# Kernel tuning notes

Hardware: AMD Instinct MI355X
Metric: run time of the kernel (lower is better)

The kernel has to match this reference:

```python
import jax, jax.numpy as jnp
import numpy as np

L, E, K, H, I = 2, 8, 2, 1024, 2048  # stack_size, num_experts, top_k, hidden, intermediate
B, S = 1, 2048


def setup_inputs() -> dict:
    key = jax.random.key(0)
    k0, k1, k2, k3 = jax.random.split(key, 4)
    hidden_states = jax.random.normal(k0, (B, S, H), dtype=jnp.float32)
    router_w = jax.random.normal(k1, (L, H, E), dtype=jnp.float32) * 0.02
    gate_up_proj = jax.random.normal(k2, (L, E, H, 2 * I), dtype=jnp.float32) * (1.0 / np.sqrt(H))
    down_proj = jax.random.normal(k3, (L, E, I, H), dtype=jnp.float32) * (1.0 / np.sqrt(I))
    return {"hidden_states": hidden_states, "router_w": router_w,
            "gate_up_proj": gate_up_proj, "down_proj": down_proj}


def _moe_layer(x, rw, gu_w, dn_w):
    # x: [T,H]; one MoE block: RouterTopK(softmax) + full-capacity top-k GLU expert MLPs
    logits = x @ rw                                   # [T,E] router linear (fp32)
    aff = jax.nn.softmax(logits, axis=-1)
    vals, idx = jax.lax.top_k(aff, K)                 # [T,K]
    vals = vals / jnp.sum(vals, axis=-1, keepdims=True)  # normalize_top_k_affinities=True
    T = x.shape[0]
    # sparse combine weights [T,E]: normalized affinity on chosen experts, 0 elsewhere
    combine = jnp.zeros((T, E), x.dtype).at[jnp.arange(T)[:, None], idx].set(vals)
    gu = jnp.einsum('th,ehi->eti', x, gu_w)           # [E,T,2I] fused gate+up per expert
    gate, up = gu[..., :I], gu[..., I:]
    act = jax.nn.silu(gate) * up                      # GLU with silu
    eo = jnp.einsum('eti,eih->eth', act, dn_w)        # [E,T,H] down proj
    out = jnp.einsum('eth,te->th', eo, combine)       # combine over experts
    return out, logits


def reference(hidden_states, router_w, gate_up_proj, down_proj):
    Bx, Sx, Hx = hidden_states.shape
    x = hidden_states.reshape(-1, Hx)                 # [T,H]
    logits_all = []
    for l in range(L):                                # fixed small stack of layers
        x, logits = _moe_layer(x, router_w[l], gate_up_proj[l], down_proj[l])
        logits_all.append(logits)
    return x.reshape(Bx, Sx, Hx), jnp.stack(logits_all)  # output, [L,T,E] router logits
```

## Files before the change

kernel.cpp:

```cpp
#include <hip/hip_runtime.h>
#include <cstdint>
#include <cstddef>

constexpr int Lc = 2, Ec = 8, Hc = 1024, Ic = 2048, Tc = 2048;

typedef __bf16 bf16x8 __attribute__((ext_vector_type(8)));
typedef float f32x4 __attribute__((ext_vector_type(4)));

__device__ __forceinline__ unsigned short f2bf(float f) {
  unsigned u = __builtin_bit_cast(unsigned, f);
  u = (u + 0x7fffu + ((u >> 16) & 1u)) >> 16;
  return (unsigned short)u;
}
__device__ __forceinline__ float bf2f(unsigned short h) {
  unsigned u = (unsigned)h << 16;
  return __builtin_bit_cast(float, u);
}
__device__ __forceinline__ bf16x8 ldfrag(const unsigned short* p) {
  return __builtin_bit_cast(bf16x8, *(const uint4*)p);
}
__device__ __forceinline__ void gl2lds(const unsigned short* g, void* lds) {
  __builtin_amdgcn_global_load_lds(
      (const __attribute__((address_space(1))) void*)g,
      (__attribute__((address_space(3))) void*)lds, 16, 0, 0);
}

__global__ void router_kernel(const float* __restrict__ x, const float* __restrict__ rw,
                              float* __restrict__ logits) {
  const int t = blockIdx.x;
  const int tid = threadIdx.x;
  float acc[Ec];
#pragma unroll
  for (int e = 0; e < Ec; ++e) acc[e] = 0.f;
  const float* xr = x + (size_t)t * Hc;
  for (int h = tid; h < Hc; h += 256) {
    const float xv = xr[h];
    const float* w = rw + (size_t)h * Ec;
#pragma unroll
    for (int e = 0; e < Ec; ++e) acc[e] += xv * w[e];
  }
  __shared__ float red[256][Ec];
#pragma unroll
  for (int e = 0; e < Ec; ++e) red[tid][e] = acc[e];
  __syncthreads();
  for (int s = 128; s > 0; s >>= 1) {
    if (tid < s) {
#pragma unroll
      for (int e = 0; e < Ec; ++e) red[tid][e] += red[tid + s][e];
    }
    __syncthreads();
  }
  if (tid < Ec) logits[(size_t)t * Ec + tid] = red[0][tid];
}

__global__ void topk_kernel(const float* __restrict__ logits, int* __restrict__ cnt,
                            int* __restrict__ tokList, float* __restrict__ wList) {
  const int t = blockIdx.x * blockDim.x + threadIdx.x;
  if (t >= Tc) return;
  float l[Ec];
#pragma unroll
  for (int e = 0; e < Ec; ++e) l[e] = logits[(size_t)t * Ec + e];
  float b0 = -3.4e38f, b1 = -3.4e38f;
  int i0 = 0, i1 = 0;
#pragma unroll
  for (int e = 0; e < Ec; ++e) {
    if (l[e] > b0) { b1 = b0; i1 = i0; b0 = l[e]; i0 = e; }
    else if (l[e] > b1) { b1 = l[e]; i1 = e; }
  }
  const float w0 = 1.f / (1.f + expf(b1 - b0));
  const float w1 = 1.f - w0;
  int p0 = atomicAdd(&cnt[i0], 1);
  tokList[i0 * Tc + p0] = t;
  wList[i0 * Tc + p0] = w0;
  int p1 = atomicAdd(&cnt[i1], 1);
  tokList[i1 * Tc + p1] = t;
  wList[i1 * Tc + p1] = w1;
}

__global__ void offsets_kernel(const int* __restrict__ cnt, int* __restrict__ off) {
  if (threadIdx.x == 0) {
    int s = 0;
    for (int e = 0; e < Ec; ++e) { off[e] = s; s += cnt[e]; }
  }
}

__global__ void convert_kernel(const float* __restrict__ x, unsigned short* __restrict__ xh,
                               unsigned short* __restrict__ xl) {
  const int i = blockIdx.x * 256 + threadIdx.x;
  const float v = x[i];
  const unsigned short h = f2bf(v);
  xh[i] = h;
  xl[i] = f2bf(v - bf2f(h));
}

template <bool SPLIT>
__global__ __launch_bounds__(256) void wconv_kernel(const float* __restrict__ src,
                                                    unsigned short* __restrict__ dh,
                                                    unsigned short* __restrict__ dl,
                                                    int K, int N) {
  const int e = blockIdx.z;
  const int n0 = blockIdx.x * 64;
  const int k0 = blockIdx.y * 64;
  const int NB = N >> 6, KS = K >> 5;
  src += (size_t)e * K * N;

  __shared__ unsigned short lh[64][66];
  __shared__ unsigned short ll[SPLIT ? 64 : 1][66];
  const int tid = threadIdx.x;

  {
    const int r = tid >> 2, cg = (tid & 3) * 16;
    const float* sp = src + (size_t)(k0 + r) * N + n0 + cg;
#pragma unroll
    for (int i = 0; i < 16; i += 4) {
      const float4 v = *(const float4*)(sp + i);
      const float f[4] = {v.x, v.y, v.z, v.w};
#pragma unroll
      for (int j = 0; j < 4; ++j) {
        const unsigned short h = f2bf(f[j]);
        lh[r][cg + i + j] = h;
        if constexpr (SPLIT) ll[r][cg + i + j] = f2bf(f[j] - bf2f(h));
      }
    }
  }
  __syncthreads();
  {
    const int ksl = tid >> 7, q = (tid >> 5) & 3, n2 = (tid & 31) * 2;
    const int kb = ksl * 32 + q * 8;
    union { unsigned short s[16]; uint4 u[2]; } oh, ol;
#pragma unroll
    for (int s = 0; s < 2; ++s)
#pragma unroll
      for (int i = 0; i < 8; ++i) {
        oh.s[s * 8 + i] = lh[kb + i][n2 + s];
        if constexpr (SPLIT) ol.s[s * 8 + i] = ll[kb + i][n2 + s];
      }
    const size_t cb =
        (((size_t)e * NB + (n0 >> 6)) * KS + (k0 >> 5) + ksl) * 2048 + q * 512 + n2 * 8;
    *(uint4*)(dh + cb) = oh.u[0];
    *(uint4*)(dh + cb + 8) = oh.u[1];
    if constexpr (SPLIT) {
      *(uint4*)(dl + cb) = ol.u[0];
      *(uint4*)(dl + cb + 8) = ol.u[1];
    }
  }
}

template <bool SPLIT>
__global__ __launch_bounds__(256) void gateup_kernel(
    const unsigned short* __restrict__ xh, const unsigned short* __restrict__ xl,
    const unsigned short* __restrict__ gwSh, const unsigned short* __restrict__ gwSl,
    const int* __restrict__ cnt, const int* __restrict__ off,
    const int* __restrict__ tokList, unsigned short* __restrict__ actH,
    unsigned short* __restrict__ actL) {
  const int d = blockIdx.x;
  const int lid = (d & 7) * ((int)gridDim.x >> 3) + (d >> 3);
  const int mi = lid & 15;
  const int e = (lid >> 4) & 7;
  const int nb = lid >> 7;
  const int M = cnt[e];
  const int m0 = mi * 128;
  if (m0 >= M) return;
  const int tid = threadIdx.x;
  const int wv = tid >> 6, l64 = tid & 63;
  const int q = l64 >> 4, mr = l64 & 15;
  const int nc = wv * 16 + mr;
  const int wvo = wv * 1024;

  __shared__ __align__(16) unsigned short sAh[2][128 * 40];
  __shared__ __align__(16) unsigned short sAl[2][SPLIT ? 128 * 40 : 8];
  __shared__ __align__(16) unsigned short sBgh[2][2048];
  __shared__ __align__(16) unsigned short sBgl[2][SPLIT ? 2048 : 8];
  __shared__ __align__(16) unsigned short sBuh[2][2048];
  __shared__ __align__(16) unsigned short sBul[2][SPLIT ? 2048 : 8];

  const size_t gBase = (((size_t)e * 64 + nb) * 32) * 2048 + tid * 8;
  const size_t uBase = (((size_t)e * 64 + nb + 32) * 32) * 2048 + tid * 8;

  const int ar = tid >> 2, ak = (tid & 3) * 8;
  int r0 = m0 + ar;      if (r0 >= M) r0 = M - 1;
  int r1 = m0 + 64 + ar; if (r1 >= M) r1 = M - 1;
  const size_t a0o = (size_t)tokList[e * Tc + r0] * Hc + ak;
  const size_t a1o = (size_t)tokList[e * Tc + r1] * Hc + ak;

  f32x4 accg[8], accu[8];
#pragma unroll
  for (int i = 0; i < 8; ++i) {
    accg[i] = f32x4{0.f, 0.f, 0.f, 0.f};
    accu[i] = f32x4{0.f, 0.f, 0.f, 0.f};
  }

  uint4 p0h = *(const uint4*)(xh + a0o);
  uint4 p1h = *(const uint4*)(xh + a1o);
  uint4 p0l, p1l;
  if constexpr (SPLIT) {
    p0l = *(const uint4*)(xl + a0o);
    p1l = *(const uint4*)(xl + a1o);
  }
  *(uint4*)&sAh[0][ar * 40 + ak] = p0h;
  *(uint4*)&sAh[0][(ar + 64) * 40 + ak] = p1h;
  if constexpr (SPLIT) {
    *(uint4*)&sAl[0][ar * 40 + ak] = p0l;
    *(uint4*)&sAl[0][(ar + 64) * 40 + ak] = p1l;
  }
  gl2lds(gwSh + gBase, (char*)sBgh[0] + wvo);
  gl2lds(gwSh + uBase, (char*)sBuh[0] + wvo);
  if constexpr (SPLIT) {
    gl2lds(gwSl + gBase, (char*)sBgl[0] + wvo);
    gl2lds(gwSl + uBase, (char*)sBul[0] + wvo);
  }
  p0h = *(const uint4*)(xh + a0o + 32);
  p1h = *(const uint4*)(xh + a1o + 32);
  if constexpr (SPLIT) {
    p0l = *(const uint4*)(xl + a0o + 32);
    p1l = *(const uint4*)(xl + a1o + 32);
  }
  __syncthreads();

#define GU_STEP(CU, NX, KS)                                                           \
  {                                                                                   \
    if ((KS) + 1 < 32) {                                                              \
      gl2lds(gwSh + gBase + (size_t)((KS) + 1) * 2048, (char*)sBgh[NX] + wvo);        \
      gl2lds(gwSh + uBase + (size_t)((KS) + 1) * 2048, (char*)sBuh[NX] + wvo);        \
      if constexpr (SPLIT) {                                                          \
        gl2lds(gwSl + gBase + (size_t)((KS) + 1) * 2048, (char*)sBgl[NX] + wvo);      \
        gl2lds(gwSl + uBase + (size_t)((KS) + 1) * 2048, (char*)sBul[NX] + wvo);      \
      }                                                                               \
      *(uint4*)&sAh[NX][ar * 40 + ak] = p0h;                                          \
      *(uint4*)&sAh[NX][(ar + 64) * 40 + ak] = p1h;                                   \
      if constexpr (SPLIT) {                                                          \
        *(uint4*)&sAl[NX][ar * 40 + ak] = p0l;                                        \
        *(uint4*)&sAl[NX][(ar + 64) * 40 + ak] = p1l;                                 \
      }                                                                               \
      if ((KS) + 2 < 32) {                                                            \
        const int ko = ((KS) + 2) * 32;                                               \
        p0h = *(const uint4*)(xh + a0o + ko);                                         \
        p1h = *(const uint4*)(xh + a1o + ko);                                         \
        if constexpr (SPLIT) {                                                        \
          p0l = *(const uint4*)(xl + a0o + ko);                                       \
          p1l = *(const uint4*)(xl + a1o + ko);                                       \
        }                                                                             \
      }                                                                               \
    }                                                                                 \
    const bf16x8 bghf = ldfrag(&sBgh[CU][(q * 64 + nc) * 8]);                         \
    const bf16x8 buhf = ldfrag(&sBuh[CU][(q * 64 + nc) * 8]);                         \
    bf16x8 bglf, bulf;                                                                \
    if constexpr (SPLIT) {                                                            \
      bglf = ldfrag(&sBgl[CU][(q * 64 + nc) * 8]);                                    \
      bulf = ldfrag(&sBul[CU][(q * 64 + nc) * 8]);                                    \
    }                                                                                 \
    _Pragma("unroll")                                                                 \
    for (int mt = 0; mt < 8; ++mt) {                                                  \
      const bf16x8 ah = ldfrag(&sAh[CU][(mt * 16 + mr) * 40 + q * 8]);                \
      accg[mt] = __builtin_amdgcn_mfma_f32_16x16x32_bf16(ah, bghf, accg[mt], 0, 0, 0);\
      accu[mt] = __builtin_amdgcn_mfma_f32_16x16x32_bf16(ah, buhf, accu[mt], 0, 0, 0);\
      if constexpr (SPLIT) {                                                          \
        const bf16x8 alr = ldfrag(&sAl[CU][(mt * 16 + mr) * 40 + q * 8]);             \
        accg[mt] = __builtin_amdgcn_mfma_f32_16x16x32_bf16(ah, bglf, accg[mt], 0, 0, 0);\
        accg[mt] = __builtin_amdgcn_mfma_f32_16x16x32_bf16(alr, bghf, accg[mt], 0, 0, 0);\
        accu[mt] = __builtin_amdgcn_mfma_f32_16x16x32_bf16(ah, bulf, accu[mt], 0, 0, 0);\
        accu[mt] = __builtin_amdgcn_mfma_f32_16x16x32_bf16(alr, buhf, accu[mt], 0, 0, 0);\
      }                                                                               \
    }                                                                                 \
    __syncthreads();                                                                  \
  }

  for (int ks = 0; ks < 32; ks += 2) {
    GU_STEP(0, 1, ks)
    GU_STEP(1, 0, ks + 1)
  }
#undef GU_STEP

  const int valid = M - m0;
  const int rowbase = off[e] + m0;
#pragma unroll
  for (int mt = 0; mt < 8; ++mt) {
#pragma unroll
    for (int r = 0; r < 4; ++r) {
      const int row = mt * 16 + q * 4 + r;
      if (row < valid) {
        const float g = accg[mt][r];
        const float u = accu[mt][r];
        const float a = (g / (1.f + expf(-g))) * u;
        const size_t idx = (size_t)(rowbase + row) * Ic + (nb * 64 + nc);
        const unsigned short h = f2bf(a);
        actH[idx] = h;
        if constexpr (SPLIT) actL[idx] = f2bf(a - bf2f(h));
      }
    }
  }
}

template <bool SPLIT>
__global__ __launch_bounds__(256) void down_kernel(
    const unsigned short* __restrict__ actH, const unsigned short* __restrict__ actL,
    const unsigned short* __restrict__ dwSh, const unsigned short* __restrict__ dwSl,
    const int* __restrict__ cnt, const int* __restrict__ off,
    const int* __restrict__ tokList, const float* __restrict__ wList,
    float* __restrict__ out) {
  const int d = blockIdx.x;
  const int lid = (d & 7) * ((int)gridDim.x >> 3) + (d >> 3);
  const int mi = lid & 15;
  const int e = (lid >> 4) & 7;
  const int nb = lid >> 7;
  const int M = cnt[e];
  const int m0 = mi * 128;
  if (m0 >= M) return;
  const int tid = threadIdx.x;
  const int wv = tid >> 6, l64 = tid & 63;
  const int q = l64 >> 4, mr = l64 & 15;
  const int nc = wv * 16 + mr;
  const int wvo = wv * 1024;

  __shared__ __align__(16) unsigned short sAh[2][128 * 40];
  __shared__ __align__(16) unsigned short sAl[2][SPLIT ? 128 * 40 : 8];
  __shared__ __align__(16) unsigned short sBh[2][2048];
  __shared__ __align__(16) unsigned short sBl[2][SPLIT ? 2048 : 8];
  __shared__ int sTok[128];
  __shared__ float sW[128];

  if (tid < 128) {
    int r = m0 + tid;
    int rc = r < M ? r : M - 1;
    sTok[tid] = tokList[e * Tc + rc];
    sW[tid] = wList[e * Tc + rc];
  }

  const size_t bBase = (((size_t)e * 16 + nb) * 64) * 2048 + tid * 8;

  const int ar = tid >> 2, ak = (tid & 3) * 8;
  int r0 = m0 + ar;      if (r0 >= M) r0 = M - 1;
  int r1 = m0 + 64 + ar; if (r1 >= M) r1 = M - 1;
  const size_t a0o = (size_t)(off[e] + r0) * Ic + ak;
  const size_t a1o = (size_t)(off[e] + r1) * Ic + ak;

  f32x4 acc[8];
#pragma unroll
  for (int i = 0; i < 8; ++i) acc[i] = f32x4{0.f, 0.f, 0.f, 0.f};

  uint4 p0h = *(const uint4*)(actH + a0o);
  uint4 p1h = *(const uint4*)(actH + a1o);
  uint4 p0l, p1l;
  if constexpr (SPLIT) {
    p0l = *(const uint4*)(actL + a0o);
    p1l = *(const uint4*)(actL + a1o);
  }
  *(uint4*)&sAh[0][ar * 40 + ak] = p0h;
  *(uint4*)&sAh[0][(ar + 64) * 40 + ak] = p1h;
  if constexpr (SPLIT) {
    *(uint4*)&sAl[0][ar * 40 + ak] = p0l;
    *(uint4*)&sAl[0][(ar + 64) * 40 + ak] = p1l;
  }
  gl2lds(dwSh + bBase, (char*)sBh[0] + wvo);
  if constexpr (SPLIT) gl2lds(dwSl + bBase, (char*)sBl[0] + wvo);
  p0h = *(const uint4*)(actH + a0o + 32);
  p1h = *(const uint4*)(actH + a1o + 32);
  if constexpr (SPLIT) {
    p0l = *(const uint4*)(actL + a0o + 32);
    p1l = *(const uint4*)(actL + a1o + 32);
  }
  __syncthreads();

#define DN_STEP(CU, NX, KS)                                                           \
  {                                                                                   \
    if ((KS) + 1 < 64) {                                                              \
      gl2lds(dwSh + bBase + (size_t)((KS) + 1) * 2048, (char*)sBh[NX] + wvo);         \
      if constexpr (SPLIT)                                                            \
        gl2lds(dwSl + bBase + (size_t)((KS) + 1) * 2048, (char*)sBl[NX] + wvo);       \
      *(uint4*)&sAh[NX][ar * 40 + ak] = p0h;                                          \
      *(uint4*)&sAh[NX][(ar + 64) * 40 + ak] = p1h;                                   \
      if constexpr (SPLIT) {                                                          \
        *(uint4*)&sAl[NX][ar * 40 + ak] = p0l;                                        \
        *(uint4*)&sAl[NX][(ar + 64) * 40 + ak] = p1l;                                 \
      }                                                                               \
      if ((KS) + 2 < 64) {                                                            \
        const int ko = ((KS) + 2) * 32;                                               \
        p0h = *(const uint4*)(actH + a0o + ko);                                       \
        p1h = *(const uint4*)(actH + a1o + ko);                                       \
        if constexpr (SPLIT) {                                                        \
          p0l = *(const uint4*)(actL + a0o + ko);                                     \
          p1l = *(const uint4*)(actL + a1o + ko);                                     \
        }                                                                             \
      }                                                                               \
    }                                                                                 \
    const bf16x8 bh = ldfrag(&sBh[CU][(q * 64 + nc) * 8]);                            \
    bf16x8 bl;                                                                        \
    if constexpr (SPLIT) bl = ldfrag(&sBl[CU][(q * 64 + nc) * 8]);                    \
    _Pragma("unroll")                                                                 \
    for (int mt = 0; mt < 8; ++mt) {                                                  \
      const bf16x8 ah = ldfrag(&sAh[CU][(mt * 16 + mr) * 40 + q * 8]);                \
      acc[mt] = __builtin_amdgcn_mfma_f32_16x16x32_bf16(ah, bh, acc[mt], 0, 0, 0);    \
      if constexpr (SPLIT) {                                                          \
        const bf16x8 alr = ldfrag(&sAl[CU][(mt * 16 + mr) * 40 + q * 8]);             \
        acc[mt] = __builtin_amdgcn_mfma_f32_16x16x32_bf16(ah, bl, acc[mt], 0, 0, 0);  \
        acc[mt] = __builtin_amdgcn_mfma_f32_16x16x32_bf16(alr, bh, acc[mt], 0, 0, 0); \
      }                                                                               \
    }                                                                                 \
    __syncthreads();                                                                  \
  }

  for (int ks = 0; ks < 64; ks += 2) {
    DN_STEP(0, 1, ks)
    DN_STEP(1, 0, ks + 1)
  }
#undef DN_STEP

  const int valid = M - m0;
#pragma unroll
  for (int mt = 0; mt < 8; ++mt) {
#pragma unroll
    for (int r = 0; r < 4; ++r) {
      const int row = mt * 16 + q * 4 + r;
      if (row < valid) {
        atomicAdd(&out[(size_t)sTok[row] * Hc + (nb * 64 + nc)], sW[row] * acc[mt][r]);
      }
    }
  }
}

extern "C" void kernel_launch(void* const* d_in, const int* in_sizes, int n_in, void* d_out,
                              int out_size, void* d_ws, size_t ws_size, hipStream_t stream) {
  const float* x_in = (const float*)d_in[0];
  const float* rw = (const float*)d_in[1];
  const float* guw = (const float*)d_in[2];
  const float* dnw = (const float*)d_in[3];
  float* out = (float*)d_out;
  float* logits_base = out + (size_t)Tc * Hc;

  uint8_t* w = (uint8_t*)d_ws;
  float* x1 = (float*)w;                    w += (size_t)Tc * Hc * 4;
  unsigned short* xh = (unsigned short*)w;  w += (size_t)Tc * Hc * 2;
  unsigned short* xl = (unsigned short*)w;  w += (size_t)Tc * Hc * 2;
  unsigned short* actH = (unsigned short*)w; w += (size_t)Tc * 2 * Ic * 2;
  unsigned short* actL = (unsigned short*)w; w += (size_t)Tc * 2 * Ic * 2;
  int* tokList = (int*)w;                   w += (size_t)Ec * Tc * 4;
  float* wList = (float*)w;                 w += (size_t)Ec * Tc * 4;
  int* cnt0 = (int*)w;                      w += 64;
  int* cnt1 = (int*)w;                      w += 64;
  int* off = (int*)w;                       w += 64;
  unsigned short* wTh = (unsigned short*)w; w += (size_t)Ec * 2 * Ic * Hc * 2;
  unsigned short* wTl = (unsigned short*)w; w += (size_t)Ec * 2 * Ic * Hc * 2;

  hipMemsetAsync(cnt0, 0, 192, stream);
  hipMemsetAsync(x1, 0, (size_t)Tc * Hc * 4, stream);
  hipMemsetAsync(out, 0, (size_t)Tc * Hc * 4, stream);

  router_kernel<<<Tc, 256, 0, stream>>>(x_in, rw, logits_base);
  topk_kernel<<<Tc / 256, 256, 0, stream>>>(logits_base, cnt0, tokList, wList);
  offsets_kernel<<<1, 64, 0, stream>>>(cnt0, off);
  convert_kernel<<<(Tc * Hc) / 256, 256, 0, stream>>>(x_in, xh, xl);
  wconv_kernel<true><<<dim3(2 * Ic / 64, Hc / 64, Ec), 256, 0, stream>>>(guw, wTh, wTl, Hc, 2 * Ic);
  gateup_kernel<true><<<16 * 32 * Ec, 256, 0, stream>>>(xh, xl, wTh, wTl, cnt0, off,
                                                        tokList, actH, actL);
  wconv_kernel<true><<<dim3(Hc / 64, Ic / 64, Ec), 256, 0, stream>>>(dnw, wTh, wTl, Ic, Hc);
  down_kernel<true><<<16 * 16 * Ec, 256, 0, stream>>>(actH, actL, wTh, wTl, cnt0,
                                                      off, tokList, wList, x1);

  const float* rw1 = rw + (size_t)Hc * Ec;
  const float* guw1 = guw + (size_t)Ec * Hc * 2 * Ic;
  const float* dnw1 = dnw + (size_t)Ec * Ic * Hc;
  router_kernel<<<Tc, 256, 0, stream>>>(x1, rw1, logits_base + (size_t)Tc * Ec);
  topk_kernel<<<Tc / 256, 256, 0, stream>>>(logits_base + (size_t)Tc * Ec, cnt1, tokList, wList);
  offsets_kernel<<<1, 64, 0, stream>>>(cnt1, off);
  convert_kernel<<<(Tc * Hc) / 256, 256, 0, stream>>>(x1, xh, xl);
  wconv_kernel<false><<<dim3(2 * Ic / 64, Hc / 64, Ec), 256, 0, stream>>>(guw1, wTh, wTl, Hc, 2 * Ic);
  gateup_kernel<false><<<16 * 32 * Ec, 256, 0, stream>>>(xh, xl, wTh, wTl, cnt1, off,
                                                         tokList, actH, actL);
  wconv_kernel<false><<<dim3(Hc / 64, Ic / 64, Ec), 256, 0, stream>>>(dnw1, wTh, wTl, Ic, Hc);
  down_kernel<false><<<16 * 16 * Ec, 256, 0, stream>>>(actH, actL, wTh, wTl, cnt1,
                                                       off, tokList, wList, out);
}
```

Baseline: 1.022 ms.

## Load GEMM A fragments directly from global to registers and fuse convert into router

```diff
diff --git a/kernel.cpp b/kernel.cpp
--- a/kernel.cpp
+++ b/kernel.cpp
@@ -19,25 +19,43 @@
 __device__ __forceinline__ bf16x8 ldfrag(const unsigned short* p) {
   return __builtin_bit_cast(bf16x8, *(const uint4*)p);
 }
+__device__ __forceinline__ bf16x8 ldfragG(const unsigned short* p) {
+  return __builtin_bit_cast(bf16x8, *(const uint4*)p);
+}
 __device__ __forceinline__ void gl2lds(const unsigned short* g, void* lds) {
   __builtin_amdgcn_global_load_lds(
       (const __attribute__((address_space(1))) void*)g,
       (__attribute__((address_space(3))) void*)lds, 16, 0, 0);
 }
 
-__global__ void router_kernel(const float* __restrict__ x, const float* __restrict__ rw,
-                              float* __restrict__ logits) {
+__global__ __launch_bounds__(256) void router_kernel(
+    const float* __restrict__ x, const float* __restrict__ rw, float* __restrict__ logits,
+    unsigned short* __restrict__ xh, unsigned short* __restrict__ xl) {
   const int t = blockIdx.x;
   const int tid = threadIdx.x;
+  const float* xr = x + (size_t)t * Hc;
+  const int h0 = tid * 4;
+  const float4 v = *(const float4*)(xr + h0);
+  const float f[4] = {v.x, v.y, v.z, v.w};
+  unsigned short hs[4], ls[4];
+#pragma unroll
+  for (int j = 0; j < 4; ++j) {
+    hs[j] = f2bf(f[j]);
+    ls[j] = f2bf(f[j] - bf2f(hs[j]));
+  }
+  *(uint2*)(xh + (size_t)t * Hc + h0) =
+      uint2{(unsigned)hs[0] | ((unsigned)hs[1] << 16), (unsigned)hs[2] | ((unsigned)hs[3] << 16)};
+  *(uint2*)(xl + (size_t)t * Hc + h0) =
+      uint2{(unsigned)ls[0] | ((unsigned)ls[1] << 16), (unsigned)ls[2] | ((unsigned)ls[3] << 16)};
+
   float acc[Ec];
 #pragma unroll
   for (int e = 0; e < Ec; ++e) acc[e] = 0.f;
-  const float* xr = x + (size_t)t * Hc;
-  for (int h = tid; h < Hc; h += 256) {
-    const float xv = xr[h];
-    const float* w = rw + (size_t)h * Ec;
-#pragma unroll
-    for (int e = 0; e < Ec; ++e) acc[e] += xv * w[e];
+#pragma unroll
+  for (int j = 0; j < 4; ++j) {
+    const float* w = rw + (size_t)(h0 + j) * Ec;
+#pragma unroll
+    for (int e = 0; e < Ec; ++e) acc[e] += f[j] * w[e];
   }
   __shared__ float red[256][Ec];
 #pragma unroll
@@ -82,15 +100,6 @@
     int s = 0;
     for (int e = 0; e < Ec; ++e) { off[e] = s; s += cnt[e]; }
   }
-}
-
-__global__ void convert_kernel(const float* __restrict__ x, unsigned short* __restrict__ xh,
-                               unsigned short* __restrict__ xl) {
-  const int i = blockIdx.x * 256 + threadIdx.x;
-  const float v = x[i];
-  const unsigned short h = f2bf(v);
-  xh[i] = h;
-  xl[i] = f2bf(v - bf2f(h));
 }
 
 template <bool SPLIT>
@@ -147,7 +156,7 @@
 }
 
 template <bool SPLIT>
-__global__ __launch_bounds__(256) void gateup_kernel(
+__global__ __launch_bounds__(256, SPLIT ? 2 : 3) void gateup_kernel(
     const unsigned short* __restrict__ xh, const unsigned short* __restrict__ xl,
     const unsigned short* __restrict__ gwSh, const unsigned short* __restrict__ gwSl,
     const int* __restrict__ cnt, const int* __restrict__ off,
@@ -167,8 +176,6 @@
   const int nc = wv * 16 + mr;
   const int wvo = wv * 1024;
 
-  __shared__ __align__(16) unsigned short sAh[2][128 * 40];
-  __shared__ __align__(16) unsigned short sAl[2][SPLIT ? 128 * 40 : 8];
   __shared__ __align__(16) unsigned short sBgh[2][2048];
   __shared__ __align__(16) unsigned short sBgl[2][SPLIT ? 2048 : 8];
   __shared__ __align__(16) unsigned short sBuh[2][2048];
@@ -177,11 +184,13 @@
   const size_t gBase = (((size_t)e * 64 + nb) * 32) * 2048 + tid * 8;
   const size_t uBase = (((size_t)e * 64 + nb + 32) * 32) * 2048 + tid * 8;
 
-  const int ar = tid >> 2, ak = (tid & 3) * 8;
-  int r0 = m0 + ar;      if (r0 >= M) r0 = M - 1;
-  int r1 = m0 + 64 + ar; if (r1 >= M) r1 = M - 1;
-  const size_t a0o = (size_t)tokList[e * Tc + r0] * Hc + ak;
-  const size_t a1o = (size_t)tokList[e * Tc + r1] * Hc + ak;
+  unsigned aoff[8];
+#pragma unroll
+  for (int mt = 0; mt < 8; ++mt) {
+    int r = m0 + mt * 16 + mr;
+    if (r >= M) r = M - 1;
+    aoff[mt] = (unsigned)tokList[e * Tc + r] * Hc + q * 8;
+  }
 
   f32x4 accg[8], accu[8];
 #pragma unroll
@@ -190,18 +199,11 @@
     accu[i] = f32x4{0.f, 0.f, 0.f, 0.f};
   }
 
-  uint4 p0h = *(const uint4*)(xh + a0o);
-  uint4 p1h = *(const uint4*)(xh + a1o);
-  uint4 p0l, p1l;
-  if constexpr (SPLIT) {
-    p0l = *(const uint4*)(xl + a0o);
-    p1l = *(const uint4*)(xl + a1o);
-  }
-  *(uint4*)&sAh[0][ar * 40 + ak] = p0h;
-  *(uint4*)&sAh[0][(ar + 64) * 40 + ak] = p1h;
-  if constexpr (SPLIT) {
-    *(uint4*)&sAl[0][ar * 40 + ak] = p0l;
-    *(uint4*)&sAl[0][(ar + 64) * 40 + ak] = p1l;
+  bf16x8 ah0[8], al0[8], ah1[8], al1[8];
+#pragma unroll
+  for (int mt = 0; mt < 8; ++mt) {
+    ah0[mt] = ldfragG(xh + aoff[mt]);
+    if constexpr (SPLIT) al0[mt] = ldfragG(xl + aoff[mt]);
   }
   gl2lds(gwSh + gBase, (char*)sBgh[0] + wvo);
   gl2lds(gwSh + uBase, (char*)sBuh[0] + wvo);
@@ -209,65 +211,50 @@
     gl2lds(gwSl + gBase, (char*)sBgl[0] + wvo);
     gl2lds(gwSl + uBase, (char*)sBul[0] + wvo);
   }
-  p0h = *(const uint4*)(xh + a0o + 32);
-  p1h = *(const uint4*)(xh + a1o + 32);
-  if constexpr (SPLIT) {
-    p0l = *(const uint4*)(xl + a0o + 32);
-    p1l = *(const uint4*)(xl + a1o + 32);
-  }
   __syncthreads();
 
-#define GU_STEP(CU, NX, KS)                                                           \
-  {                                                                                   \
-    if ((KS) + 1 < 32) {                                                              \
-      gl2lds(gwSh + gBase + (size_t)((KS) + 1) * 2048, (char*)sBgh[NX] + wvo);        \
-      gl2lds(gwSh + uBase + (size_t)((KS) + 1) * 2048, (char*)sBuh[NX] + wvo);        \
-      if constexpr (SPLIT) {                                                          \
-        gl2lds(gwSl + gBase + (size_t)((KS) + 1) * 2048, (char*)sBgl[NX] + wvo);      \
-        gl2lds(gwSl + uBase + (size_t)((KS) + 1) * 2048, (char*)sBul[NX] + wvo);      \
-      }                                                                               \
-      *(uint4*)&sAh[NX][ar * 40 + ak] = p0h;                                          \
-      *(uint4*)&sAh[NX][(ar + 64) * 40 + ak] = p1h;                                   \
-      if constexpr (SPLIT) {                                                          \
-        *(uint4*)&sAl[NX][ar * 40 + ak] = p0l;                                        \
-        *(uint4*)&sAl[NX][(ar + 64) * 40 + ak] = p1l;                                 \
-      }                                                                               \
-      if ((KS) + 2 < 32) {                                                            \
-        const int ko = ((KS) + 2) * 32;                                               \
-        p0h = *(const uint4*)(xh + a0o + ko);                                         \
-        p1h = *(const uint4*)(xh + a1o + ko);                                         \
-        if constexpr (SPLIT) {                                                        \
-          p0l = *(const uint4*)(xl + a0o + ko);                                       \
-          p1l = *(const uint4*)(xl + a1o + ko);                                       \
-        }                                                                             \
-      }                                                                               \
-    }                                                                                 \
-    const bf16x8 bghf = ldfrag(&sBgh[CU][(q * 64 + nc) * 8]);                         \
-    const bf16x8 buhf = ldfrag(&sBuh[CU][(q * 64 + nc) * 8]);                         \
-    bf16x8 bglf, bulf;                                                                \
-    if constexpr (SPLIT) {                                                            \
-      bglf = ldfrag(&sBgl[CU][(q * 64 + nc) * 8]);                                    \
-      bulf = ldfrag(&sBul[CU][(q * 64 + nc) * 8]);                                    \
-    }                                                                                 \
-    _Pragma("unroll")                                                                 \
-    for (int mt = 0; mt < 8; ++mt) {                                                  \
-      const bf16x8 ah = ldfrag(&sAh[CU][(mt * 16 + mr) * 40 + q * 8]);                \
-      accg[mt] = __builtin_amdgcn_mfma_f32_16x16x32_bf16(ah, bghf, accg[mt], 0, 0, 0);\
-      accu[mt] = __builtin_amdgcn_mfma_f32_16x16x32_bf16(ah, buhf, accu[mt], 0, 0, 0);\
-      if constexpr (SPLIT) {                                                          \
-        const bf16x8 alr = ldfrag(&sAl[CU][(mt * 16 + mr) * 40 + q * 8]);             \
-        accg[mt] = __builtin_amdgcn_mfma_f32_16x16x32_bf16(ah, bglf, accg[mt], 0, 0, 0);\
-        accg[mt] = __builtin_amdgcn_mfma_f32_16x16x32_bf16(alr, bghf, accg[mt], 0, 0, 0);\
-        accu[mt] = __builtin_amdgcn_mfma_f32_16x16x32_bf16(ah, bulf, accu[mt], 0, 0, 0);\
-        accu[mt] = __builtin_amdgcn_mfma_f32_16x16x32_bf16(alr, buhf, accu[mt], 0, 0, 0);\
-      }                                                                               \
-    }                                                                                 \
-    __syncthreads();                                                                  \
+#define GU_STEP(CU, NX, AH, AL, AHN, ALN, KS)                                           \
+  {                                                                                     \
+    if ((KS) + 1 < 32) {                                                                \
+      gl2lds(gwSh + gBase + (size_t)((KS) + 1) * 2048, (char*)sBgh[NX] + wvo);          \
+      gl2lds(gwSh + uBase + (size_t)((KS) + 1) * 2048, (char*)sBuh[NX] + wvo);          \
+      if constexpr (SPLIT) {                                                            \
+        gl2lds(gwSl + gBase + (size_t)((KS) + 1) * 2048, (char*)sBgl[NX] + wvo);        \
+        gl2lds(gwSl + uBase + (size_t)((KS) + 1) * 2048, (char*)sBul[NX] + wvo);        \
+      }                                                                                 \
+      _Pragma("unroll")                                                                 \
+      for (int mt = 0; mt < 8; ++mt) {                                                  \
+        AHN[mt] = ldfragG(xh + aoff[mt] + ((KS) + 1) * 32);                             \
+        if constexpr (SPLIT) ALN[mt] = ldfragG(xl + aoff[mt] + ((KS) + 1) * 32);        \
+      }                                                                                 \
+    }                                                                                   \
+    const bf16x8 bghf = ldfrag(&sBgh[CU][(q * 64 + nc) * 8]);                           \
+    const bf16x8 buhf = ldfrag(&sBuh[CU][(q * 64 + nc) * 8]);                           \
+    _Pragma("unroll")                                                                   \
+    for (int mt = 0; mt < 8; ++mt) {                                                    \
+      accg[mt] = __builtin_amdgcn_mfma_f32_16x16x32_bf16(AH[mt], bghf, accg[mt], 0, 0, 0); \
+      accu[mt] = __builtin_amdgcn_mfma_f32_16x16x32_bf16(AH[mt], buhf, accu[mt], 0, 0, 0); \
+    }                                                                                   \
+    if constexpr (SPLIT) {                                                              \
+      const bf16x8 bglf = ldfrag(&sBgl[CU][(q * 64 + nc) * 8]);                         \
+      const bf16x8 bulf = ldfrag(&sBul[CU][(q * 64 + nc) * 8]);                         \
+      _Pragma("unroll")                                                                 \
+      for (int mt = 0; mt < 8; ++mt) {                                                  \
+        accg[mt] = __builtin_amdgcn_mfma_f32_16x16x32_bf16(AH[mt], bglf, accg[mt], 0, 0, 0); \
+        accu[mt] = __builtin_amdgcn_mfma_f32_16x16x32_bf16(AH[mt], bulf, accu[mt], 0, 0, 0); \
+      }                                                                                 \
+      _Pragma("unroll")                                                                 \
+      for (int mt = 0; mt < 8; ++mt) {                                                  \
+        accg[mt] = __builtin_amdgcn_mfma_f32_16x16x32_bf16(AL[mt], bghf, accg[mt], 0, 0, 0); \
+        accu[mt] = __builtin_amdgcn_mfma_f32_16x16x32_bf16(AL[mt], buhf, accu[mt], 0, 0, 0); \
+      }                                                                                 \
+    }                                                                                   \
+    __syncthreads();                                                                    \
   }
 
   for (int ks = 0; ks < 32; ks += 2) {
-    GU_STEP(0, 1, ks)
-    GU_STEP(1, 0, ks + 1)
+    GU_STEP(0, 1, ah0, al0, ah1, al1, ks)
+    GU_STEP(1, 0, ah1, al1, ah0, al0, ks + 1)
   }
 #undef GU_STEP
 
@@ -292,7 +279,7 @@
 }
 
 template <bool SPLIT>
-__global__ __launch_bounds__(256) void down_kernel(
+__global__ __launch_bounds__(256, SPLIT ? 2 : 3) void down_kernel(
     const unsigned short* __restrict__ actH, const unsigned short* __restrict__ actL,
     const unsigned short* __restrict__ dwSh, const unsigned short* __restrict__ dwSl,
     const int* __restrict__ cnt, const int* __restrict__ off,
@@ -312,8 +299,6 @@
   const int nc = wv * 16 + mr;
   const int wvo = wv * 1024;
 
-  __shared__ __align__(16) unsigned short sAh[2][128 * 40];
-  __shared__ __align__(16) unsigned short sAl[2][SPLIT ? 128 * 40 : 8];
   __shared__ __align__(16) unsigned short sBh[2][2048];
   __shared__ __align__(16) unsigned short sBl[2][SPLIT ? 2048 : 8];
   __shared__ int sTok[128];
@@ -327,81 +312,61 @@
   }
 
   const size_t bBase = (((size_t)e * 16 + nb) * 64) * 2048 + tid * 8;
-
-  const int ar = tid >> 2, ak = (tid & 3) * 8;
-  int r0 = m0 + ar;      if (r0 >= M) r0 = M - 1;
-  int r1 = m0 + 64 + ar; if (r1 >= M) r1 = M - 1;
-  const size_t a0o = (size_t)(off[e] + r0) * Ic + ak;
-  const size_t a1o = (size_t)(off[e] + r1) * Ic + ak;
+  const int offE = off[e];
+
+  unsigned aoff[8];
+#pragma unroll
+  for (int mt = 0; mt < 8; ++mt) {
+    int r = m0 + mt * 16 + mr;
+    if (r >= M) r = M - 1;
+    aoff[mt] = (unsigned)(offE + r) * Ic + q * 8;
+  }
 
   f32x4 acc[8];
 #pragma unroll
   for (int i = 0; i < 8; ++i) acc[i] = f32x4{0.f, 0.f, 0.f, 0.f};
 
-  uint4 p0h = *(const uint4*)(actH + a0o);
-  uint4 p1h = *(const uint4*)(actH + a1o);
-  uint4 p0l, p1l;
-  if constexpr (SPLIT) {
-    p0l = *(const uint4*)(actL + a0o);
-    p1l = *(const uint4*)(actL + a1o);
-  }
-  *(uint4*)&sAh[0][ar * 40 + ak] = p0h;
-  *(uint4*)&sAh[0][(ar + 64) * 40 + ak] = p1h;
-  if constexpr (SPLIT) {
-    *(uint4*)&sAl[0][ar * 40 + ak] = p0l;
-    *(uint4*)&sAl[0][(ar + 64) * 40 + ak] = p1l;
+  bf16x8 ah0[8], al0[8], ah1[8], al1[8];
+#pragma unroll
+  for (int mt = 0; mt < 8; ++mt) {
+    ah0[mt] = ldfragG(actH + aoff[mt]);
+    if constexpr (SPLIT) al0[mt] = ldfragG(actL + aoff[mt]);
   }
   gl2lds(dwSh + bBase, (char*)sBh[0] + wvo);
   if constexpr (SPLIT) gl2lds(dwSl + bBase, (char*)sBl[0] + wvo);
-  p0h = *(const uint4*)(actH + a0o + 32);
-  p1h = *(const uint4*)(actH + a1o + 32);
-  if constexpr (SPLIT) {
-    p0l = *(const uint4*)(actL + a0o + 32);
-    p1l = *(const uint4*)(actL + a1o + 32);
-  }
   __syncthreads();
 
-#define DN_STEP(CU, NX, KS)                                                           \
-  {                                                                                   \
-    if ((KS) + 1 < 64) {                                                              \
-      gl2lds(dwSh + bBase + (size_t)((KS) + 1) * 2048, (char*)sBh[NX] + wvo);         \
-      if constexpr (SPLIT)                                                            \
-        gl2lds(dwSl + bBase + (size_t)((KS) + 1) * 2048, (char*)sBl[NX] + wvo);       \
-      *(uint4*)&sAh[NX][ar * 40 + ak] = p0h;                                          \
-      *(uint4*)&sAh[NX][(ar + 64) * 40 + ak] = p1h;                                   \
-      if constexpr (SPLIT) {                                                          \
-        *(uint4*)&sAl[NX][ar * 40 + ak] = p0l;                                        \
-        *(uint4*)&sAl[NX][(ar + 64) * 40 + ak] = p1l;                                 \
-      }                                                                               \
-      if ((KS) + 2 < 64) {                                                            \
-        const int ko = ((KS) + 2) * 32;                                               \
-        p0h = *(const uint4*)(actH + a0o + ko);                                       \
-        p1h = *(const uint4*)(actH + a1o + ko);                                       \
-        if constexpr (SPLIT) {                                                        \
-          p0l = *(const uint4*)(actL + a0o + ko);                                     \
-          p1l = *(const uint4*)(actL + a1o + ko);                                     \
-        }                                                                             \
-      }                                                                               \
-    }                                                                                 \
-    const bf16x8 bh = ldfrag(&sBh[CU][(q * 64 + nc) * 8]);                            \
-    bf16x8 bl;                                                                        \
-    if constexpr (SPLIT) bl = ldfrag(&sBl[CU][(q * 64 + nc) * 8]);                    \
-    _Pragma("unroll")                                                                 \
-    for (int mt = 0; mt < 8; ++mt) {                                                  \
-      const bf16x8 ah = ldfrag(&sAh[CU][(mt * 16 + mr) * 40 + q * 8]);                \
-      acc[mt] = __builtin_amdgcn_mfma_f32_16x16x32_bf16(ah, bh, acc[mt], 0, 0, 0);    \
-      if constexpr (SPLIT) {                                                          \
-        const bf16x8 alr = ldfrag(&sAl[CU][(mt * 16 + mr) * 40 + q * 8]);             \
-        acc[mt] = __builtin_amdgcn_mfma_f32_16x16x32_bf16(ah, bl, acc[mt], 0, 0, 0);  \
-        acc[mt] = __builtin_amdgcn_mfma_f32_16x16x32_bf16(alr, bh, acc[mt], 0, 0, 0); \
-      }                                                                               \
-    }                                                                                 \
-    __syncthreads();                                                                  \
+#define DN_STEP(CU, NX, AH, AL, AHN, ALN, KS)                                           \
+  {                                                                                     \
+    if ((KS) + 1 < 64) {                                                                \
+      gl2lds(dwSh + bBase + (size_t)((KS) + 1) * 2048, (char*)sBh[NX] + wvo);           \
+      if constexpr (SPLIT)                                                              \
+        gl2lds(dwSl + bBase + (size_t)((KS) + 1) * 2048, (char*)sBl[NX] + wvo);         \
+      _Pragma("unroll")                                                                 \
+      for (int mt = 0; mt < 8; ++mt) {                                                  \
+        AHN[mt] = ldfragG(actH + aoff[mt] + ((KS) + 1) * 32);                           \
+        if constexpr (SPLIT) ALN[mt] = ldfragG(actL + aoff[mt] + ((KS) + 1) * 32);      \
+      }                                                                                 \
+    }                                                                                   \
+    const bf16x8 bh = ldfrag(&sBh[CU][(q * 64 + nc) * 8]);                              \
+    _Pragma("unroll")                                                                   \
+    for (int mt = 0; mt < 8; ++mt)                                                      \
+      acc[mt] = __builtin_amdgcn_mfma_f32_16x16x32_bf16(AH[mt], bh, acc[mt], 0, 0, 0);  \
+    if constexpr (SPLIT) {                                                              \
+      const bf16x8 bl = ldfrag(&sBl[CU][(q * 64 + nc) * 8]);                            \
+      _Pragma("unroll")                                                                 \
+      for (int mt = 0; mt < 8; ++mt)                                                    \
+        acc[mt] = __builtin_amdgcn_mfma_f32_16x16x32_bf16(AH[mt], bl, acc[mt], 0, 0, 0);\
+      _Pragma("unroll")                                                                 \
+      for (int mt = 0; mt < 8; ++mt)                                                    \
+        acc[mt] = __builtin_amdgcn_mfma_f32_16x16x32_bf16(AL[mt], bh, acc[mt], 0, 0, 0);\
+    }                                                                                   \
+    __syncthreads();                                                                    \
   }
 
   for (int ks = 0; ks < 64; ks += 2) {
-    DN_STEP(0, 1, ks)
-    DN_STEP(1, 0, ks + 1)
+    DN_STEP(0, 1, ah0, al0, ah1, al1, ks)
+    DN_STEP(1, 0, ah1, al1, ah0, al0, ks + 1)
   }
 #undef DN_STEP
 
@@ -445,10 +410,9 @@
   hipMemsetAsync(x1, 0, (size_t)Tc * Hc * 4, stream);
   hipMemsetAsync(out, 0, (size_t)Tc * Hc * 4, stream);
 
-  router_kernel<<<Tc, 256, 0, stream>>>(x_in, rw, logits_base);
+  router_kernel<<<Tc, 256, 0, stream>>>(x_in, rw, logits_base, xh, xl);
   topk_kernel<<<Tc / 256, 256, 0, stream>>>(logits_base, cnt0, tokList, wList);
   offsets_kernel<<<1, 64, 0, stream>>>(cnt0, off);
-  convert_kernel<<<(Tc * Hc) / 256, 256, 0, stream>>>(x_in, xh, xl);
   wconv_kernel<true><<<dim3(2 * Ic / 64, Hc / 64, Ec), 256, 0, stream>>>(guw, wTh, wTl, Hc, 2 * Ic);
   gateup_kernel<true><<<16 * 32 * Ec, 256, 0, stream>>>(xh, xl, wTh, wTl, cnt0, off,
                                                         tokList, actH, actL);
@@ -459,10 +423,9 @@
   const float* rw1 = rw + (size_t)Hc * Ec;
   const float* guw1 = guw + (size_t)Ec * Hc * 2 * Ic;
   const float* dnw1 = dnw + (size_t)Ec * Ic * Hc;
-  router_kernel<<<Tc, 256, 0, stream>>>(x1, rw1, logits_base + (size_t)Tc * Ec);
+  router_kernel<<<Tc, 256, 0, stream>>>(x1, rw1, logits_base + (size_t)Tc * Ec, xh, xl);
   topk_kernel<<<Tc / 256, 256, 0, stream>>>(logits_base + (size_t)Tc * Ec, cnt1, tokList, wList);
   offsets_kernel<<<1, 64, 0, stream>>>(cnt1, off);
-  convert_kernel<<<(Tc * Hc) / 256, 256, 0, stream>>>(x1, xh, xl);
   wconv_kernel<false><<<dim3(2 * Ic / 64, Hc / 64, Ec), 256, 0, stream>>>(guw1, wTh, wTl, Hc, 2 * Ic);
   gateup_kernel<false><<<16 * 32 * Ec, 256, 0, stream>>>(xh, xl, wTh, wTl, cnt1, off,
                                                          tokList, actH, actL);
```

Result: slower. 1.786 ms (+74.7%).
